# Performance work log

Measured on AMD Instinct MI355X. Metric: run time of the kernel, lower is better.

The kernel has to match this reference:

```python
import jax, jax.numpy as jnp
import numpy as np

D = 32          # d_model
OUT = 2         # output_dim ('binding', 'radius')
PMAX = 118      # static max proton count (replaces data-dependent amax)
NMAX = 236     # static max neutron count
B = 1 << 20


def setup_inputs() -> dict:
    key = jax.random.key(0)
    ks = jax.random.split(key, 16)
    protons = jax.random.randint(ks[0], (B,), 1, PMAX + 1, dtype=jnp.int32)
    neutrons = jax.random.randint(ks[1], (B,), 1, NMAX + 1, dtype=jnp.int32)
    x = jnp.stack([protons, neutrons], axis=1)  # [B, 2]
    s = 1.0 / np.sqrt(D)
    inp = {
        "x": x,
        "embeddings": jax.random.normal(ks[2], (2, D), jnp.float32) * s,
        "Wp": jax.random.normal(ks[3], (D, D), jnp.float32) * s,
        "bp": jax.random.normal(ks[4], (D,), jnp.float32) * s,
        "Wn": jax.random.normal(ks[5], (D, D), jnp.float32) * s,
        "bn": jax.random.normal(ks[6], (D,), jnp.float32) * s,
        "W1": jax.random.normal(ks[7], (D, 2 * D), jnp.float32) * (1.0 / np.sqrt(2 * D)),
        "b1": jax.random.normal(ks[8], (D,), jnp.float32) * s,
        "ln_g": jnp.ones((D,), jnp.float32),
        "ln_b": jnp.zeros((D,), jnp.float32),
        "W2": jax.random.normal(ks[9], (D, D), jnp.float32) * s,
        "b2": jax.random.normal(ks[10], (D,), jnp.float32) * s,
        "Wr": jax.random.normal(ks[11], (OUT, D), jnp.float32) * s,
        "br": jax.random.normal(ks[12], (OUT,), jnp.float32) * s,
    }
    return inp


def _silu(v):
    return v * jax.nn.sigmoid(v)


def _chain(W, b, p0, length):
    # sequential recurrence p_t = Linear(SiLU(p_{t-1})); stack all states
    def step(p, _):
        p = _silu(p) @ W.T + b
        return p, p
    _, states = jax.lax.scan(step, p0, None, length=length)
    return states  # [length, D]


def _layernorm(h, g, b, eps=1e-5):
    mu = jnp.mean(h, axis=-1, keepdims=True)
    var = jnp.mean(jnp.square(h - mu), axis=-1, keepdims=True)
    return (h - mu) * jax.lax.rsqrt(var + eps) * g + b


def reference(x, embeddings, Wp, bp, Wn, bn, W1, b1, ln_g, ln_b, W2, b2, Wr, br):
    p_states = _chain(Wp, bp, embeddings[0], PMAX)   # [PMAX, D]
    n_states = _chain(Wn, bn, embeddings[1], NMAX)   # [NMAX, D]
    pf = p_states[x[:, 0] - 1]                       # [B, D]
    nf = n_states[x[:, 1] - 1]                       # [B, D]
    h = jnp.concatenate([pf, nf], axis=1)            # [B, 2D]
    h = h @ W1.T + b1                                # Linear(2D -> D)
    h = _silu(h)
    h = _layernorm(h, ln_g, ln_b)
    h = h @ W2.T + b2                                # Linear(D -> D)
    return h @ Wr.T + br                             # readout [B, OUT]
```

## Files before the change

kernel.cpp:

```cpp
#include <hip/hip_runtime.h>
#include <hip/hip_bf16.h>

#define DD 32
#define P_MAX 118
#define N_MAX 236
#define TBL (P_MAX * N_MAX)

typedef int   ivec4 __attribute__((ext_vector_type(4)));
typedef float fvec4 __attribute__((ext_vector_type(4)));

#define PST 0
#define NST (P_MAX * DD)
#define UOF ((P_MAX + N_MAX) * DD)
#define VOF (UOF + DD * P_MAX)
#define TOF (VOF + DD * N_MAX)

__global__ __launch_bounds__(64) void chain_kernel(
    const float* __restrict__ emb,
    const float* __restrict__ Wp, const float* __restrict__ bp,
    const float* __restrict__ Wn, const float* __restrict__ bn,
    float* __restrict__ ws)
{
    const int lane = threadIdx.x;
    const int ch = lane & 31;

    const float* W;
    const float* b;
    const float* e0;
    float* out;
    int len;
    if (blockIdx.x == 0) {
        W = Wp; b = bp; e0 = emb;       out = ws + PST; len = P_MAX;
    } else {
        W = Wn; b = bn; e0 = emb + DD;  out = ws + NST; len = N_MAX;
    }

    float w[32];
#pragma unroll
    for (int q = 0; q < 8; ++q) {
        float4 v = reinterpret_cast<const float4*>(W + ch * 32)[q];
        w[4 * q + 0] = v.x; w[4 * q + 1] = v.y;
        w[4 * q + 2] = v.z; w[4 * q + 3] = v.w;
    }
    const float bias = b[ch];
    float p = e0[ch];

    for (int t = 0; t < len; ++t) {
        float e = __expf(-p);
        float s = p * __builtin_amdgcn_rcpf(1.0f + e);
        int sb = __float_as_int(s);

        float a0 = 0.0f, a1 = 0.0f, a2 = 0.0f, a3 = 0.0f;
#pragma unroll
        for (int k = 0; k < 32; k += 4) {
            a0 += __int_as_float(__builtin_amdgcn_readlane(sb, k + 0)) * w[k + 0];
            a1 += __int_as_float(__builtin_amdgcn_readlane(sb, k + 1)) * w[k + 1];
            a2 += __int_as_float(__builtin_amdgcn_readlane(sb, k + 2)) * w[k + 2];
            a3 += __int_as_float(__builtin_amdgcn_readlane(sb, k + 3)) * w[k + 3];
        }
        p = bias + ((a0 + a1) + (a2 + a3));
        if (lane < 32) out[t * DD + ch] = p;
    }
}

__global__ __launch_bounds__(64) void uv_kernel(
    const float* __restrict__ ws_in,
    const float* __restrict__ W1, const float* __restrict__ b1,
    float* __restrict__ ws_out)
{
    const int j = blockIdx.y;
    const int bx = blockIdx.x;
    const int lane = threadIdx.x;
    const bool prot = bx < 2;
    const int t = prot ? bx * 64 + lane : (bx - 2) * 64 + lane;
    const int len = prot ? P_MAX : N_MAX;
    if (t >= len) return;

    const float* st = ws_in + (prot ? PST : NST) + t * DD;
    const float* wr = W1 + j * 64 + (prot ? 0 : 32);
    float acc = prot ? 0.0f : b1[j];
#pragma unroll
    for (int q = 0; q < 8; ++q) {
        float4 s4 = reinterpret_cast<const float4*>(st)[q];
        acc = fmaf(s4.x, wr[4 * q + 0], acc);
        acc = fmaf(s4.y, wr[4 * q + 1], acc);
        acc = fmaf(s4.z, wr[4 * q + 2], acc);
        acc = fmaf(s4.w, wr[4 * q + 3], acc);
    }
    if (prot) ws_out[UOF + j * P_MAX + t] = acc;
    else      ws_out[VOF + j * N_MAX + t] = acc;
}

__global__ __launch_bounds__(64, 1) void table_kernel(
    const float* __restrict__ ws,
    const float* __restrict__ ln_g, const float* __restrict__ ln_b,
    const float* __restrict__ W2, const float* __restrict__ b2,
    const float* __restrict__ Wr, const float* __restrict__ br,
    float2* __restrict__ table)
{
    const int e = blockIdx.x * 64 + threadIdx.x;
    if (e >= TBL) return;
    const int pi = e / N_MAX;
    const int ni = e - pi * N_MAX;

    const float* UT = ws + UOF;
    const float* VT = ws + VOF;

    float h[32];
    float mu = 0.0f;
#pragma unroll
    for (int j = 0; j < 32; ++j) {
        float a = UT[j * P_MAX + pi] + VT[j * N_MAX + ni];
        float ee = __expf(-a);
        float s = a * __builtin_amdgcn_rcpf(1.0f + ee);
        h[j] = s;
        mu += s;
    }
    mu *= (1.0f / 32.0f);
    float var = 0.0f;
#pragma unroll
    for (int j = 0; j < 32; ++j) {
        float d = h[j] - mu;
        var = fmaf(d, d, var);
    }
    var *= (1.0f / 32.0f);
    const float inv = __builtin_amdgcn_rsqf(var + 1e-5f);
#pragma unroll
    for (int j = 0; j < 32; ++j)
        h[j] = (h[j] - mu) * inv * ln_g[j] + ln_b[j];

    float h2[32];
#pragma unroll
    for (int j0 = 0; j0 < 32; j0 += 8) {
        float acc[8];
#pragma unroll
        for (int u = 0; u < 8; ++u) acc[u] = b2[j0 + u];
#pragma unroll
        for (int k = 0; k < 32; ++k) {
#pragma unroll
            for (int u = 0; u < 8; ++u)
                acc[u] = fmaf(h[k], W2[(j0 + u) * 32 + k], acc[u]);
        }
#pragma unroll
        for (int u = 0; u < 8; ++u) h2[j0 + u] = acc[u];
    }

    float o0 = br[0], o1 = br[1];
    float p0 = 0.0f, p1 = 0.0f;
#pragma unroll
    for (int k = 0; k < 32; k += 2) {
        o0 = fmaf(h2[k], Wr[k], o0);
        p0 = fmaf(h2[k + 1], Wr[k + 1], p0);
        o1 = fmaf(h2[k], Wr[32 + k], o1);
        p1 = fmaf(h2[k + 1], Wr[32 + k + 1], p1);
    }
    table[e] = make_float2(o0 + p0, o1 + p1);
}

__global__ __launch_bounds__(256) void gather_kernel(
    const ivec4* __restrict__ x4,
    const float2* __restrict__ table,
    fvec4* __restrict__ out4,
    int B4)
{
    const int i = blockIdx.x * 256 + threadIdx.x;
    if (i >= B4) return;
    ivec4 a = __builtin_nontemporal_load(x4 + 2 * i);
    ivec4 b = __builtin_nontemporal_load(x4 + 2 * i + 1);
    float2 t0 = table[(a.x - 1) * N_MAX + (a.y - 1)];
    float2 t1 = table[(a.z - 1) * N_MAX + (a.w - 1)];
    float2 t2 = table[(b.x - 1) * N_MAX + (b.y - 1)];
    float2 t3 = table[(b.z - 1) * N_MAX + (b.w - 1)];
    fvec4 o0v = {t0.x, t0.y, t1.x, t1.y};
    fvec4 o1v = {t2.x, t2.y, t3.x, t3.y};
    __builtin_nontemporal_store(o0v, out4 + 2 * i);
    __builtin_nontemporal_store(o1v, out4 + 2 * i + 1);
}

extern "C" void kernel_launch(void* const* d_in, const int* in_sizes, int n_in,
                              void* d_out, int out_size, void* d_ws, size_t ws_size,
                              hipStream_t stream) {
    const int*   x    = (const int*)d_in[0];
    const float* emb  = (const float*)d_in[1];
    const float* Wp   = (const float*)d_in[2];
    const float* bp   = (const float*)d_in[3];
    const float* Wn   = (const float*)d_in[4];
    const float* bn   = (const float*)d_in[5];
    const float* W1   = (const float*)d_in[6];
    const float* b1   = (const float*)d_in[7];
    const float* ln_g = (const float*)d_in[8];
    const float* ln_b = (const float*)d_in[9];
    const float* W2   = (const float*)d_in[10];
    const float* b2   = (const float*)d_in[11];
    const float* Wr   = (const float*)d_in[12];
    const float* br   = (const float*)d_in[13];

    const int B = in_sizes[0] / 2;

    float* wsf = (float*)d_ws;
    float2* table = (float2*)(wsf + TOF);

    chain_kernel<<<2, 64, 0, stream>>>(emb, Wp, bp, Wn, bn, wsf);

    uv_kernel<<<dim3(6, 32), 64, 0, stream>>>(wsf, W1, b1, wsf);

    table_kernel<<<(TBL + 63) / 64, 64, 0, stream>>>(
        wsf, ln_g, ln_b, W2, b2, Wr, br, table);

    gather_kernel<<<(B / 4 + 255) / 256, 256, 0, stream>>>(
        (const ivec4*)x, table, (fvec4*)d_out, B / 4);
}
```

Before: 139.9 us.

## Fuse uv, table and gather stages into one cooperative grid-synced kernel

Merges the W1 projection, the 118x236 lookup-table build and the batch gather into a single cooperative kernel, with grid-wide syncs between the stages. The gather becomes a grid-stride loop over a fixed 512x256 grid. The goal is to remove two kernel launches and their inter-kernel gaps. In exchange it adds grid.sync barriers and threadfences, lowers gather parallelism to a fixed grid, and depends on the cooperative launch being able to place all blocks at once.

```diff
diff --git a/kernel.cpp b/kernel.cpp
--- a/kernel.cpp
+++ b/kernel.cpp
@@ -1,5 +1,8 @@
 #include <hip/hip_runtime.h>
 #include <hip/hip_bf16.h>
+#include <hip/hip_cooperative_groups.h>
+
+namespace cg = cooperative_groups;
 
 #define DD 32
 #define P_MAX 118
@@ -14,6 +17,10 @@
 #define UOF ((P_MAX + N_MAX) * DD)
 #define VOF (UOF + DD * P_MAX)
 #define TOF (VOF + DD * N_MAX)
+
+#define FGRID 512
+#define FBLK  256
+#define FTHREADS (FGRID * FBLK)
 
 __global__ __launch_bounds__(64) void chain_kernel(
     const float* __restrict__ emb,
@@ -63,118 +70,125 @@
     }
 }
 
-__global__ __launch_bounds__(64) void uv_kernel(
-    const float* __restrict__ ws_in,
+__global__ __launch_bounds__(FBLK, 2) void fused_kernel(
     const float* __restrict__ W1, const float* __restrict__ b1,
-    float* __restrict__ ws_out)
-{
-    const int j = blockIdx.y;
-    const int bx = blockIdx.x;
-    const int lane = threadIdx.x;
-    const bool prot = bx < 2;
-    const int t = prot ? bx * 64 + lane : (bx - 2) * 64 + lane;
-    const int len = prot ? P_MAX : N_MAX;
-    if (t >= len) return;
-
-    const float* st = ws_in + (prot ? PST : NST) + t * DD;
-    const float* wr = W1 + j * 64 + (prot ? 0 : 32);
-    float acc = prot ? 0.0f : b1[j];
-#pragma unroll
-    for (int q = 0; q < 8; ++q) {
-        float4 s4 = reinterpret_cast<const float4*>(st)[q];
-        acc = fmaf(s4.x, wr[4 * q + 0], acc);
-        acc = fmaf(s4.y, wr[4 * q + 1], acc);
-        acc = fmaf(s4.z, wr[4 * q + 2], acc);
-        acc = fmaf(s4.w, wr[4 * q + 3], acc);
-    }
-    if (prot) ws_out[UOF + j * P_MAX + t] = acc;
-    else      ws_out[VOF + j * N_MAX + t] = acc;
-}
-
-__global__ __launch_bounds__(64, 1) void table_kernel(
-    const float* __restrict__ ws,
     const float* __restrict__ ln_g, const float* __restrict__ ln_b,
     const float* __restrict__ W2, const float* __restrict__ b2,
     const float* __restrict__ Wr, const float* __restrict__ br,
-    float2* __restrict__ table)
-{
-    const int e = blockIdx.x * 64 + threadIdx.x;
-    if (e >= TBL) return;
-    const int pi = e / N_MAX;
-    const int ni = e - pi * N_MAX;
-
-    const float* UT = ws + UOF;
-    const float* VT = ws + VOF;
-
-    float h[32];
-    float mu = 0.0f;
-#pragma unroll
-    for (int j = 0; j < 32; ++j) {
-        float a = UT[j * P_MAX + pi] + VT[j * N_MAX + ni];
-        float ee = __expf(-a);
-        float s = a * __builtin_amdgcn_rcpf(1.0f + ee);
-        h[j] = s;
-        mu += s;
-    }
-    mu *= (1.0f / 32.0f);
-    float var = 0.0f;
-#pragma unroll
-    for (int j = 0; j < 32; ++j) {
-        float d = h[j] - mu;
-        var = fmaf(d, d, var);
-    }
-    var *= (1.0f / 32.0f);
-    const float inv = __builtin_amdgcn_rsqf(var + 1e-5f);
-#pragma unroll
-    for (int j = 0; j < 32; ++j)
-        h[j] = (h[j] - mu) * inv * ln_g[j] + ln_b[j];
-
-    float h2[32];
-#pragma unroll
-    for (int j0 = 0; j0 < 32; j0 += 8) {
-        float acc[8];
-#pragma unroll
-        for (int u = 0; u < 8; ++u) acc[u] = b2[j0 + u];
-#pragma unroll
-        for (int k = 0; k < 32; ++k) {
-#pragma unroll
-            for (int u = 0; u < 8; ++u)
-                acc[u] = fmaf(h[k], W2[(j0 + u) * 32 + k], acc[u]);
-        }
-#pragma unroll
-        for (int u = 0; u < 8; ++u) h2[j0 + u] = acc[u];
-    }
-
-    float o0 = br[0], o1 = br[1];
-    float p0 = 0.0f, p1 = 0.0f;
-#pragma unroll
-    for (int k = 0; k < 32; k += 2) {
-        o0 = fmaf(h2[k], Wr[k], o0);
-        p0 = fmaf(h2[k + 1], Wr[k + 1], p0);
-        o1 = fmaf(h2[k], Wr[32 + k], o1);
-        p1 = fmaf(h2[k + 1], Wr[32 + k + 1], p1);
-    }
-    table[e] = make_float2(o0 + p0, o1 + p1);
-}
-
-__global__ __launch_bounds__(256) void gather_kernel(
     const ivec4* __restrict__ x4,
-    const float2* __restrict__ table,
+    float* __restrict__ ws,
     fvec4* __restrict__ out4,
     int B4)
 {
-    const int i = blockIdx.x * 256 + threadIdx.x;
-    if (i >= B4) return;
-    ivec4 a = __builtin_nontemporal_load(x4 + 2 * i);
-    ivec4 b = __builtin_nontemporal_load(x4 + 2 * i + 1);
-    float2 t0 = table[(a.x - 1) * N_MAX + (a.y - 1)];
-    float2 t1 = table[(a.z - 1) * N_MAX + (a.w - 1)];
-    float2 t2 = table[(b.x - 1) * N_MAX + (b.y - 1)];
-    float2 t3 = table[(b.z - 1) * N_MAX + (b.w - 1)];
-    fvec4 o0v = {t0.x, t0.y, t1.x, t1.y};
-    fvec4 o1v = {t2.x, t2.y, t3.x, t3.y};
-    __builtin_nontemporal_store(o0v, out4 + 2 * i);
-    __builtin_nontemporal_store(o1v, out4 + 2 * i + 1);
+    cg::grid_group grid = cg::this_grid();
+    const int tid = blockIdx.x * FBLK + threadIdx.x;
+
+    {
+        const int wv = (blockIdx.x << 2) | (threadIdx.x >> 6);
+        if (wv < 192) {
+            const int lane = threadIdx.x & 63;
+            const int j  = wv / 6;
+            const int bx = wv - 6 * j;
+            const bool prot = bx < 2;
+            const int t = prot ? bx * 64 + lane : (bx - 2) * 64 + lane;
+            const int len = prot ? P_MAX : N_MAX;
+            if (t < len) {
+                const float* st = ws + (prot ? PST : NST) + t * DD;
+                const float* wr = W1 + j * 64 + (prot ? 0 : 32);
+                float acc = prot ? 0.0f : b1[j];
+#pragma unroll
+                for (int q = 0; q < 8; ++q) {
+                    float4 s4 = reinterpret_cast<const float4*>(st)[q];
+                    acc = fmaf(s4.x, wr[4 * q + 0], acc);
+                    acc = fmaf(s4.y, wr[4 * q + 1], acc);
+                    acc = fmaf(s4.z, wr[4 * q + 2], acc);
+                    acc = fmaf(s4.w, wr[4 * q + 3], acc);
+                }
+                if (prot) ws[UOF + j * P_MAX + t] = acc;
+                else      ws[VOF + j * N_MAX + t] = acc;
+            }
+        }
+    }
+
+    __threadfence();
+    grid.sync();
+
+    float2* table = (float2*)(ws + TOF);
+    if (tid < TBL) {
+        const int e = tid;
+        const int pi = e / N_MAX;
+        const int ni = e - pi * N_MAX;
+
+        const float* UT = ws + UOF;
+        const float* VT = ws + VOF;
+
+        float h[32];
+        float mu = 0.0f;
+#pragma unroll
+        for (int j = 0; j < 32; ++j) {
+            float a = UT[j * P_MAX + pi] + VT[j * N_MAX + ni];
+            float ee = __expf(-a);
+            float s = a * __builtin_amdgcn_rcpf(1.0f + ee);
+            h[j] = s;
+            mu += s;
+        }
+        mu *= (1.0f / 32.0f);
+        float var = 0.0f;
+#pragma unroll
+        for (int j = 0; j < 32; ++j) {
+            float d = h[j] - mu;
+            var = fmaf(d, d, var);
+        }
+        var *= (1.0f / 32.0f);
+        const float inv = __builtin_amdgcn_rsqf(var + 1e-5f);
+#pragma unroll
+        for (int j = 0; j < 32; ++j)
+            h[j] = (h[j] - mu) * inv * ln_g[j] + ln_b[j];
+
+        float h2[32];
+#pragma unroll
+        for (int j0 = 0; j0 < 32; j0 += 8) {
+            float acc[8];
+#pragma unroll
+            for (int u = 0; u < 8; ++u) acc[u] = b2[j0 + u];
+#pragma unroll
+            for (int k = 0; k < 32; ++k) {
+#pragma unroll
+                for (int u = 0; u < 8; ++u)
+                    acc[u] = fmaf(h[k], W2[(j0 + u) * 32 + k], acc[u]);
+            }
+#pragma unroll
+            for (int u = 0; u < 8; ++u) h2[j0 + u] = acc[u];
+        }
+
+        float o0 = br[0], o1 = br[1];
+        float p0 = 0.0f, p1 = 0.0f;
+#pragma unroll
+        for (int k = 0; k < 32; k += 2) {
+            o0 = fmaf(h2[k], Wr[k], o0);
+            p0 = fmaf(h2[k + 1], Wr[k + 1], p0);
+            o1 = fmaf(h2[k], Wr[32 + k], o1);
+            p1 = fmaf(h2[k + 1], Wr[32 + k + 1], p1);
+        }
+        table[e] = make_float2(o0 + p0, o1 + p1);
+    }
+
+    __threadfence();
+    grid.sync();
+
+    const float2* tbl = (const float2*)(ws + TOF);
+    for (int i = tid; i < B4; i += FTHREADS) {
+        ivec4 a = __builtin_nontemporal_load(x4 + 2 * i);
+        ivec4 b = __builtin_nontemporal_load(x4 + 2 * i + 1);
+        float2 t0 = tbl[(a.x - 1) * N_MAX + (a.y - 1)];
+        float2 t1 = tbl[(a.z - 1) * N_MAX + (a.w - 1)];
+        float2 t2 = tbl[(b.x - 1) * N_MAX + (b.y - 1)];
+        float2 t3 = tbl[(b.z - 1) * N_MAX + (b.w - 1)];
+        fvec4 o0v = {t0.x, t0.y, t1.x, t1.y};
+        fvec4 o1v = {t2.x, t2.y, t3.x, t3.y};
+        __builtin_nontemporal_store(o0v, out4 + 2 * i);
+        __builtin_nontemporal_store(o1v, out4 + 2 * i + 1);
+    }
 }
 
 extern "C" void kernel_launch(void* const* d_in, const int* in_sizes, int n_in,
@@ -196,17 +210,19 @@
     const float* br   = (const float*)d_in[13];
 
     const int B = in_sizes[0] / 2;
+    int B4 = B / 4;
 
     float* wsf = (float*)d_ws;
-    float2* table = (float2*)(wsf + TOF);
 
     chain_kernel<<<2, 64, 0, stream>>>(emb, Wp, bp, Wn, bn, wsf);
 
-    uv_kernel<<<dim3(6, 32), 64, 0, stream>>>(wsf, W1, b1, wsf);
-
-    table_kernel<<<(TBL + 63) / 64, 64, 0, stream>>>(
-        wsf, ln_g, ln_b, W2, b2, Wr, br, table);
-
-    gather_kernel<<<(B / 4 + 255) / 256, 256, 0, stream>>>(
-        (const ivec4*)x, table, (fvec4*)d_out, B / 4);
+    const ivec4* x4 = (const ivec4*)x;
+    fvec4* out4 = (fvec4*)d_out;
+    void* args[] = {
+        (void*)&W1, (void*)&b1, (void*)&ln_g, (void*)&ln_b,
+        (void*)&W2, (void*)&b2, (void*)&Wr, (void*)&br,
+        (void*)&x4, (void*)&wsf, (void*)&out4, (void*)&B4
+    };
+    hipLaunchCooperativeKernel((void*)fused_kernel, dim3(FGRID), dim3(FBLK),
+                               args, 0, stream);
 }
```

Measured after the change: 341.6 us. 2.44x slower.
